# Performance work log

Hardware: AMD Instinct MI355X
Metric: run time of the kernel (lower is better)

The kernel has to match this reference:

```python
import jax, jax.numpy as jnp
import numpy as np

IN_F = 4096
OUT_F = 4096
N_TOK = 8192
MAX_ITER = IN_F * OUT_F // 2  # default max_iter=-1 -> half of weight entries


def _approx_matmul(x, weight, max_iter):
    """Budgeted approximate matmul: only the `max_iter` largest-magnitude
    weight entries participate (the rest of the multiply-accumulate budget is
    skipped). Faithful to the iteration-budget semantics of Approx_Matmul:
    max_iter multiply-adds out of in_features*out_features total.
    """
    n = weight.size
    flat_abs = jnp.abs(weight).reshape(-1)
    # threshold = k-th largest magnitude (static k -> jit-friendly)
    kth = jnp.sort(flat_abs)[n - max_iter]
    mask = (jnp.abs(weight) >= kth).astype(weight.dtype)
    w_eff = weight * jax.lax.stop_gradient(mask)
    # y[t, o] = sum_i x[t, i] * w_eff[o, i]
    return jnp.einsum('ti,oi->to', x, w_eff)


def setup_inputs() -> dict:
    key = jax.random.key(0)
    kx, kw, kb = jax.random.split(key, 3)
    x = jax.random.normal(kx, (N_TOK, IN_F), dtype=jnp.float32)
    # kaiming_uniform_(a=sqrt(5)) on [out, in] -> bound = 1/sqrt(in_features)
    bound = 1.0 / np.sqrt(IN_F)
    weight = jax.random.uniform(kw, (OUT_F, IN_F), dtype=jnp.float32,
                                minval=-bound, maxval=bound)
    bias = jax.random.uniform(kb, (OUT_F,), dtype=jnp.float32,
                              minval=-bound, maxval=bound)
    return {"x": x, "weight": weight, "bias": bias}


def reference(x, weight, bias):
    mid = _approx_matmul(x, weight, MAX_ITER)
    return mid + bias
```

## Files before the change

kernel.cpp:

```cpp
#include <hip/hip_runtime.h>

#define IN_F   4096
#define OUT_F  4096
#define N_TOK  8192
#define NW     (OUT_F * IN_F)
#define SEL_TARGET 8388608u

typedef unsigned int  u32;
typedef unsigned short u16;

typedef __bf16 bf16x8 __attribute__((ext_vector_type(8)));
typedef float  f32x4  __attribute__((ext_vector_type(4)));

__device__ inline u16 f2bf_rne(float f) {
    u32 u = __float_as_uint(f);
    u32 r = (u + 0x7fffu + ((u >> 16) & 1u)) >> 16;
    return (u16)r;
}

template <int PASS>
__global__ void hist_kernel(const uint4* __restrict__ wb,
                            u32* __restrict__ hist,
                            const u32* __restrict__ scal) {
    constexpr int NB = (PASS == 1) ? 2048 : 1024;
    __shared__ u32 lh[NB];
    for (int i = threadIdx.x; i < NB; i += blockDim.x) lh[i] = 0;
    u32 pfx = (PASS == 1) ? 0u : scal[0];
    __syncthreads();

    const int nvec = NW / 4;
    const int stride = gridDim.x * blockDim.x;
    for (int i = blockIdx.x * blockDim.x + threadIdx.x; i < nvec; i += stride) {
        uint4 v = wb[i];
        u32 k[4] = {v.x & 0x7fffffffu, v.y & 0x7fffffffu,
                    v.z & 0x7fffffffu, v.w & 0x7fffffffu};
        #pragma unroll
        for (int j = 0; j < 4; j++) {
            if (PASS == 1) {
                atomicAdd(&lh[k[j] >> 20], 1u);
            } else if (PASS == 2) {
                if ((k[j] >> 20) == pfx) atomicAdd(&lh[(k[j] >> 10) & 1023u], 1u);
            } else {
                if ((k[j] >> 10) == pfx) atomicAdd(&lh[k[j] & 1023u], 1u);
            }
        }
    }
    __syncthreads();
    for (int i = threadIdx.x; i < NB; i += blockDim.x)
        if (lh[i]) atomicAdd(&hist[i], lh[i]);
}

template <int PASS>
__global__ void find_kernel(const u32* __restrict__ hist, u32* __restrict__ scal) {
    constexpr int NB  = (PASS == 1) ? 2048 : 1024;
    constexpr int PER = NB / 256;
    __shared__ u32 tgt_s;
    __shared__ u32 part[256];
    int t = threadIdx.x;
    if (t == 0) tgt_s = (PASS == 1) ? SEL_TARGET : scal[1];
    __syncthreads();
    u32 target = tgt_s;

    u32 loc[PER];
    u32 s = 0;
    #pragma unroll
    for (int i = 0; i < PER; i++) { loc[i] = hist[t * PER + i]; s += loc[i]; }
    part[t] = s;
    __syncthreads();
    #pragma unroll
    for (int off = 1; off < 256; off <<= 1) {
        u32 v = (t >= off) ? part[t - off] : 0u;
        __syncthreads();
        part[t] += v;
        __syncthreads();
    }
    u32 cum = (t == 0) ? 0u : part[t - 1];
    #pragma unroll
    for (int i = 0; i < PER; i++) {
        u32 h = loc[i];
        if (target >= cum && target < cum + h) {
            u32 bin = (u32)(t * PER + i);
            if (PASS == 1)      { scal[0] = bin;                       scal[1] = target - cum; }
            else if (PASS == 2) { scal[0] = (scal[0] << 10) | bin;     scal[1] = target - cum; }
            else                { scal[2] = (scal[0] << 10) | bin; }
        }
        cum += h;
    }
}

__global__ void convert_w_kernel(const uint4* __restrict__ wb,
                                 u16* __restrict__ w16,
                                 const u32* __restrict__ scal) {
    const u32 kth = scal[2];
    const int nvec = NW / 4;
    const int stride = gridDim.x * blockDim.x;
    for (int i = blockIdx.x * blockDim.x + threadIdx.x; i < nvec; i += stride) {
        uint4 v = wb[i];
        ushort4 o;
        o.x = ((v.x & 0x7fffffffu) >= kth) ? f2bf_rne(__uint_as_float(v.x)) : (u16)0;
        o.y = ((v.y & 0x7fffffffu) >= kth) ? f2bf_rne(__uint_as_float(v.y)) : (u16)0;
        o.z = ((v.z & 0x7fffffffu) >= kth) ? f2bf_rne(__uint_as_float(v.z)) : (u16)0;
        o.w = ((v.w & 0x7fffffffu) >= kth) ? f2bf_rne(__uint_as_float(v.w)) : (u16)0;
        *(ushort4*)&w16[(size_t)i * 4] = o;
    }
}

__global__ void convert_x_kernel(const float4* __restrict__ xb,
                                 u16* __restrict__ x16) {
    const int nvec = (N_TOK * IN_F) / 4;
    const int stride = gridDim.x * blockDim.x;
    for (int i = blockIdx.x * blockDim.x + threadIdx.x; i < nvec; i += stride) {
        float4 v = xb[i];
        ushort4 o;
        o.x = f2bf_rne(v.x);
        o.y = f2bf_rne(v.y);
        o.z = f2bf_rne(v.z);
        o.w = f2bf_rne(v.w);
        *(ushort4*)&x16[(size_t)i * 4] = o;
    }
}

#define BK 64
#define NT (IN_F / BK)

#define ASLOT(buf, ks) (((buf) * 2 + (ks)) * 8192)
#define BSLOT(buf, ks) (32768 + ((buf) * 2 + (ks)) * 8192)

#define VMCNT(n) asm volatile("s_waitcnt vmcnt(" #n ")" ::: "memory")
#define LGKM0    asm volatile("s_waitcnt lgkmcnt(0)" ::: "memory")
#define SB0      __builtin_amdgcn_sched_barrier(0)
#define BARR()   __builtin_amdgcn_s_barrier()

__global__ __launch_bounds__(512, 2) void gemm8p(
    const u16* __restrict__ A,
    const u16* __restrict__ B,
    const float* __restrict__ bias,
    float* __restrict__ C) {
    __shared__ u16 lds[65536];

    const int tid  = threadIdx.x;
    const int lane = tid & 63;
    const int ln15 = lane & 15;
    const int l16  = lane >> 4;
    const int wv   = tid >> 6;
    const int wr   = wv >> 2;
    const int wc   = wv & 3;
    const int wrow = wr * 128;
    const int wcol = wc * 64;

    const int bid = blockIdx.x;
    const int swz = (bid & 7) * 64 + (bid >> 3);
    const int by  = swz >> 4;
    const int bx  = swz & 15;
    const int arow = by * 256;
    const int brow = bx * 256;

    f32x4 acc[8][4];
    #pragma unroll
    for (int m = 0; m < 8; m++)
        #pragma unroll
        for (int n = 0; n < 4; n++)
            acc[m][n] = {0.f, 0.f, 0.f, 0.f};

    #define STAGE(G, rowbase, kt, ks, slot) do {                                        \
        _Pragma("unroll")                                                               \
        for (int i_ = 0; i_ < 2; i_++) {                                                \
            int q_  = tid + i_ * 512;                                                   \
            int r_  = q_ >> 2;                                                          \
            int cs_ = (q_ & 3) ^ ((r_ >> 1) & 3);                                       \
            const u16* src_ = (G) + (size_t)((rowbase) + r_) * IN_F                     \
                              + (kt) * BK + (ks) * 32 + cs_ * 8;                        \
            __builtin_amdgcn_global_load_lds(                                           \
                (const __attribute__((address_space(1))) unsigned int*)src_,            \
                (__attribute__((address_space(3))) unsigned int*)&lds[(slot) + q_ * 8], \
                16, 0, 0);                                                              \
        } } while (0)

    #define READ_A(mh, ks, buf) do {                                                    \
        _Pragma("unroll")                                                               \
        for (int i_ = 0; i_ < 4; i_++) {                                                \
            int row_ = wrow + ((mh) * 4 + i_) * 16 + ln15;                              \
            int cc_  = l16 ^ ((row_ >> 1) & 3);                                         \
            aF[i_] = *(const bf16x8*)&lds[ASLOT(buf, ks) + row_ * 32 + cc_ * 8];        \
        } } while (0)

    #define READ_B(ks, buf) do {                                                       \
        _Pragma("unroll")                                                               \
        for (int i_ = 0; i_ < 4; i_++) {                                                \
            int row_ = wcol + i_ * 16 + ln15;                                           \
            int cc_  = l16 ^ ((row_ >> 1) & 3);                                         \
            bF[i_] = *(const bf16x8*)&lds[BSLOT(buf, ks) + row_ * 32 + cc_ * 8];        \
        } } while (0)

    #define MFMAQ(mh) do {                                                              \
        __builtin_amdgcn_s_setprio(1);                                                  \
        _Pragma("unroll")                                                               \
        for (int i_ = 0; i_ < 4; i_++)                                                  \
            _Pragma("unroll")                                                           \
            for (int n_ = 0; n_ < 4; n_++)                                              \
                acc[(mh) * 4 + i_][n_] = __builtin_amdgcn_mfma_f32_16x16x32_bf16(       \
                    aF[i_], bF[n_], acc[(mh) * 4 + i_][n_], 0, 0, 0);                   \
        __builtin_amdgcn_s_setprio(0);                                                  \
    } while (0)

    STAGE(B, brow, 0, 0, BSLOT(0, 0));
    STAGE(A, arow, 0, 0, ASLOT(0, 0));
    STAGE(B, brow, 0, 1, BSLOT(0, 1));
    STAGE(A, arow, 0, 1, ASLOT(0, 1));
    VMCNT(4);
    STAGE(B, brow, 1, 0, BSLOT(1, 0));
    STAGE(A, arow, 1, 0, ASLOT(1, 0));
    STAGE(B, brow, 1, 1, BSLOT(1, 1));
    VMCNT(6);
    BARR();

    bf16x8 aF[4], bF[4];

    #pragma unroll 1
    for (int it = 0; it < NT / 2; it++) {
        const int t0 = 2 * it;
        const int ka = t0 + 1;
        const int kb = (t0 + 2 < NT) ? t0 + 2 : NT - 1;
        const int kc = (t0 + 3 < NT) ? t0 + 3 : NT - 1;

        READ_A(0, 0, 0); READ_B(0, 0);
        STAGE(A, arow, ka, 1, ASLOT(1, 1));
        BARR(); LGKM0; SB0; MFMAQ(0); SB0; BARR();
        READ_A(1, 0, 0);
        STAGE(B, brow, kb, 0, BSLOT(0, 0));
        BARR(); LGKM0; SB0; MFMAQ(1); SB0; BARR();
        READ_A(0, 1, 0); READ_B(1, 0);
        STAGE(A, arow, kb, 0, ASLOT(0, 0));
        BARR(); LGKM0; SB0; MFMAQ(0); SB0; BARR();
        READ_A(1, 1, 0);
        STAGE(B, brow, kb, 1, BSLOT(0, 1));
        VMCNT(6);
        BARR(); LGKM0; SB0; MFMAQ(1); SB0; BARR();

        READ_A(0, 0, 1); READ_B(0, 1);
        STAGE(A, arow, kb, 1, ASLOT(0, 1));
        BARR(); LGKM0; SB0; MFMAQ(0); SB0; BARR();
        READ_A(1, 0, 1);
        STAGE(B, brow, kc, 0, BSLOT(1, 0));
        BARR(); LGKM0; SB0; MFMAQ(1); SB0; BARR();
        READ_A(0, 1, 1); READ_B(1, 1);
        STAGE(A, arow, kc, 0, ASLOT(1, 0));
        BARR(); LGKM0; SB0; MFMAQ(0); SB0; BARR();
        READ_A(1, 1, 1);
        STAGE(B, brow, kc, 1, BSLOT(1, 1));
        VMCNT(6);
        BARR(); LGKM0; SB0; MFMAQ(1); SB0; BARR();
    }
    VMCNT(0);

    const int cr = l16 * 4;
    #pragma unroll
    for (int n = 0; n < 4; n++) {
        int col = brow + wcol + n * 16 + ln15;
        float bv = bias[col];
        #pragma unroll
        for (int m = 0; m < 8; m++) {
            int r0 = arow + wrow + m * 16 + cr;
            #pragma unroll
            for (int j = 0; j < 4; j++) {
                C[(size_t)(r0 + j) * OUT_F + col] = acc[m][n][j] + bv;
            }
        }
    }
}

extern "C" void kernel_launch(void* const* d_in, const int* in_sizes, int n_in,
                              void* d_out, int out_size, void* d_ws, size_t ws_size,
                              hipStream_t stream) {
    const float* x    = (const float*)d_in[0];
    const float* w    = (const float*)d_in[1];
    const float* bias = (const float*)d_in[2];
    float* out = (float*)d_out;

    char* ws = (char*)d_ws;
    u32* hist1 = (u32*)(ws + 0);
    u32* hist2 = (u32*)(ws + 8192);
    u32* hist3 = (u32*)(ws + 12288);
    u32* scal  = (u32*)(ws + 16384);
    u16* w16   = (u16*)(ws + 65536);
    u16* x16   = (u16*)(ws + 65536 + (size_t)NW * 2);

    hipMemsetAsync(ws, 0, 65536, stream);

    hist_kernel<1><<<2048, 256, 0, stream>>>((const uint4*)w, hist1, scal);
    find_kernel<1><<<1, 256, 0, stream>>>(hist1, scal);
    hist_kernel<2><<<2048, 256, 0, stream>>>((const uint4*)w, hist2, scal);
    find_kernel<2><<<1, 256, 0, stream>>>(hist2, scal);
    hist_kernel<3><<<2048, 256, 0, stream>>>((const uint4*)w, hist3, scal);
    find_kernel<3><<<1, 256, 0, stream>>>(hist3, scal);

    convert_w_kernel<<<2048, 256, 0, stream>>>((const uint4*)w, w16, scal);
    convert_x_kernel<<<2048, 256, 0, stream>>>((const float4*)x, x16);

    gemm8p<<<512, 512, 0, stream>>>(x16, w16, bias, out);
}
```

Baseline: 401.9 us.

## Replace three-pass radix select with 14-bit histogram plus candidate compaction

The k-th largest magnitude threshold was found with three full histogram passes over the 64MB weight. It is now found with one pass over a 16K-bin histogram, one compaction pass that copies the values in the selected bin into a candidate buffer, and a single-block two-level select over those candidates. This removes one full read of the weights and two launches. It relies on the selected bin holding at most 1M candidates, and the compaction uses a single global atomic counter, which could contend heavily if the bin is large.

Measured after the change: 1.558 ms. 3.88x slower.

```diff
diff --git a/kernel.cpp b/kernel.cpp
--- a/kernel.cpp
+++ b/kernel.cpp
@@ -5,6 +5,7 @@
 #define N_TOK  8192
 #define NW     (OUT_F * IN_F)
 #define SEL_TARGET 8388608u
+#define CAND_CAP (1u << 20)
 
 typedef unsigned int  u32;
 typedef unsigned short u16;
@@ -18,16 +19,60 @@
     return (u16)r;
 }
 
-template <int PASS>
-__global__ void hist_kernel(const uint4* __restrict__ wb,
-                            u32* __restrict__ hist,
-                            const u32* __restrict__ scal) {
-    constexpr int NB = (PASS == 1) ? 2048 : 1024;
-    __shared__ u32 lh[NB];
-    for (int i = threadIdx.x; i < NB; i += blockDim.x) lh[i] = 0;
-    u32 pfx = (PASS == 1) ? 0u : scal[0];
-    __syncthreads();
-
+__global__ __launch_bounds__(1024) void hist1_kernel(const uint4* __restrict__ wb,
+                                                     u32* __restrict__ hist) {
+    __shared__ u32 lh[16384];
+    for (int i = threadIdx.x; i < 16384; i += 1024) lh[i] = 0;
+    __syncthreads();
+
+    const int nvec = NW / 4;
+    const int stride = gridDim.x * 1024;
+    for (int i = blockIdx.x * 1024 + threadIdx.x; i < nvec; i += stride) {
+        uint4 v = wb[i];
+        atomicAdd(&lh[(v.x & 0x7fffffffu) >> 17], 1u);
+        atomicAdd(&lh[(v.y & 0x7fffffffu) >> 17], 1u);
+        atomicAdd(&lh[(v.z & 0x7fffffffu) >> 17], 1u);
+        atomicAdd(&lh[(v.w & 0x7fffffffu) >> 17], 1u);
+    }
+    __syncthreads();
+    for (int i = threadIdx.x; i < 16384; i += 1024)
+        if (lh[i]) atomicAdd(&hist[i], lh[i]);
+}
+
+__global__ __launch_bounds__(1024) void find1_kernel(const u32* __restrict__ hist,
+                                                     u32* __restrict__ scal) {
+    __shared__ u32 part[1024];
+    const int t = threadIdx.x;
+    u32 loc[16];
+    u32 s = 0;
+    #pragma unroll
+    for (int i = 0; i < 16; i++) { loc[i] = hist[t * 16 + i]; s += loc[i]; }
+    part[t] = s;
+    __syncthreads();
+    #pragma unroll
+    for (int off = 1; off < 1024; off <<= 1) {
+        u32 v = (t >= off) ? part[t - off] : 0u;
+        __syncthreads();
+        part[t] += v;
+        __syncthreads();
+    }
+    u32 cum = (t == 0) ? 0u : part[t - 1];
+    const u32 target = SEL_TARGET;
+    #pragma unroll
+    for (int i = 0; i < 16; i++) {
+        u32 h = loc[i];
+        if (target >= cum && target < cum + h) {
+            scal[0] = (u32)(t * 16 + i);
+            scal[1] = target - cum;
+        }
+        cum += h;
+    }
+}
+
+__global__ void compact_kernel(const uint4* __restrict__ wb,
+                               u32* __restrict__ cand,
+                               u32* __restrict__ scal) {
+    const u32 pfx = scal[0];
     const int nvec = NW / 4;
     const int stride = gridDim.x * blockDim.x;
     for (int i = blockIdx.x * blockDim.x + threadIdx.x; i < nvec; i += stride) {
@@ -36,55 +81,63 @@
                     v.z & 0x7fffffffu, v.w & 0x7fffffffu};
         #pragma unroll
         for (int j = 0; j < 4; j++) {
-            if (PASS == 1) {
-                atomicAdd(&lh[k[j] >> 20], 1u);
-            } else if (PASS == 2) {
-                if ((k[j] >> 20) == pfx) atomicAdd(&lh[(k[j] >> 10) & 1023u], 1u);
-            } else {
-                if ((k[j] >> 10) == pfx) atomicAdd(&lh[k[j] & 1023u], 1u);
+            if ((k[j] >> 17) == pfx) {
+                u32 idx = atomicAdd(&scal[3], 1u);
+                if (idx < CAND_CAP) cand[idx] = k[j];
             }
         }
     }
-    __syncthreads();
-    for (int i = threadIdx.x; i < NB; i += blockDim.x)
-        if (lh[i]) atomicAdd(&hist[i], lh[i]);
-}
-
-template <int PASS>
-__global__ void find_kernel(const u32* __restrict__ hist, u32* __restrict__ scal) {
-    constexpr int NB  = (PASS == 1) ? 2048 : 1024;
-    constexpr int PER = NB / 256;
-    __shared__ u32 tgt_s;
-    __shared__ u32 part[256];
-    int t = threadIdx.x;
-    if (t == 0) tgt_s = (PASS == 1) ? SEL_TARGET : scal[1];
-    __syncthreads();
-    u32 target = tgt_s;
-
-    u32 loc[PER];
-    u32 s = 0;
-    #pragma unroll
-    for (int i = 0; i < PER; i++) { loc[i] = hist[t * PER + i]; s += loc[i]; }
-    part[t] = s;
-    __syncthreads();
-    #pragma unroll
-    for (int off = 1; off < 256; off <<= 1) {
+}
+
+__global__ __launch_bounds__(1024) void select3_kernel(const u32* __restrict__ cand,
+                                                       u32* __restrict__ scal) {
+    __shared__ u32 h2[2048];
+    __shared__ u32 part[1024];
+    __shared__ u32 h3[64];
+    __shared__ u32 sh[2];
+    const int t = threadIdx.x;
+    const u32 n = min(scal[3], CAND_CAP);
+    const u32 tgt = scal[1];
+
+    for (int i = t; i < 2048; i += 1024) h2[i] = 0;
+    __syncthreads();
+    for (u32 i = t; i < n; i += 1024)
+        atomicAdd(&h2[(cand[i] >> 6) & 2047u], 1u);
+    __syncthreads();
+
+    u32 a0 = h2[t * 2], a1 = h2[t * 2 + 1];
+    part[t] = a0 + a1;
+    __syncthreads();
+    #pragma unroll
+    for (int off = 1; off < 1024; off <<= 1) {
         u32 v = (t >= off) ? part[t - off] : 0u;
         __syncthreads();
         part[t] += v;
         __syncthreads();
     }
     u32 cum = (t == 0) ? 0u : part[t - 1];
-    #pragma unroll
-    for (int i = 0; i < PER; i++) {
-        u32 h = loc[i];
-        if (target >= cum && target < cum + h) {
-            u32 bin = (u32)(t * PER + i);
-            if (PASS == 1)      { scal[0] = bin;                       scal[1] = target - cum; }
-            else if (PASS == 2) { scal[0] = (scal[0] << 10) | bin;     scal[1] = target - cum; }
-            else                { scal[2] = (scal[0] << 10) | bin; }
+    if (tgt >= cum && tgt < cum + a0) { sh[0] = (u32)(t * 2);     sh[1] = tgt - cum; }
+    cum += a0;
+    if (tgt >= cum && tgt < cum + a1) { sh[0] = (u32)(t * 2 + 1); sh[1] = tgt - cum; }
+    __syncthreads();
+    const u32 b2 = sh[0], tgt2 = sh[1];
+
+    if (t < 64) h3[t] = 0;
+    __syncthreads();
+    for (u32 i = t; i < n; i += 1024) {
+        u32 k = cand[i];
+        if (((k >> 6) & 2047u) == b2) atomicAdd(&h3[k & 63u], 1u);
+    }
+    __syncthreads();
+    if (t == 0) {
+        u32 c = 0;
+        #pragma unroll
+        for (int b = 0; b < 64; b++) {
+            u32 h = h3[b];
+            if (tgt2 >= c && tgt2 < c + h)
+                scal[2] = (scal[0] << 17) | (b2 << 6) | (u32)b;
+            c += h;
         }
-        cum += h;
     }
 }
 
@@ -278,21 +331,19 @@
     float* out = (float*)d_out;
 
     char* ws = (char*)d_ws;
-    u32* hist1 = (u32*)(ws + 0);
-    u32* hist2 = (u32*)(ws + 8192);
-    u32* hist3 = (u32*)(ws + 12288);
-    u32* scal  = (u32*)(ws + 16384);
+    u32* scal  = (u32*)(ws + 0);
     u16* w16   = (u16*)(ws + 65536);
     u16* x16   = (u16*)(ws + 65536 + (size_t)NW * 2);
-
-    hipMemsetAsync(ws, 0, 65536, stream);
-
-    hist_kernel<1><<<2048, 256, 0, stream>>>((const uint4*)w, hist1, scal);
-    find_kernel<1><<<1, 256, 0, stream>>>(hist1, scal);
-    hist_kernel<2><<<2048, 256, 0, stream>>>((const uint4*)w, hist2, scal);
-    find_kernel<2><<<1, 256, 0, stream>>>(hist2, scal);
-    hist_kernel<3><<<2048, 256, 0, stream>>>((const uint4*)w, hist3, scal);
-    find_kernel<3><<<1, 256, 0, stream>>>(hist3, scal);
+    u32* hist16k = (u32*)x16;
+    u32* cand    = (u32*)((char*)x16 + 131072);
+
+    hipMemsetAsync(scal, 0, 64, stream);
+    hipMemsetAsync(hist16k, 0, 65536, stream);
+
+    hist1_kernel<<<256, 1024, 0, stream>>>((const uint4*)w, hist16k);
+    find1_kernel<<<1, 1024, 0, stream>>>(hist16k, scal);
+    compact_kernel<<<2048, 256, 0, stream>>>((const uint4*)w, cand, scal);
+    select3_kernel<<<1, 1024, 0, stream>>>(cand, scal);
 
     convert_w_kernel<<<2048, 256, 0, stream>>>((const uint4*)w, w16, scal);
     convert_x_kernel<<<2048, 256, 0, stream>>>((const float4*)x, x16);
```
